# Performance work log

Measured on AMD Instinct MI355X. Metric: run time of the kernel, lower is better.

## Reference

```python
import jax, jax.numpy as jnp
import numpy as np

B, S, D = 2, 400, 512  # batch, seq (src == tgt for self-attention), dim; attn_hidden=0 so d == D


def setup_inputs() -> dict:
    key = jax.random.key(0)
    ks = jax.random.split(key, 9)
    inv = 1.0 / np.sqrt(D)
    return {
        "input": jax.random.normal(ks[0], (B, S, D), jnp.float32),
        "memory_bank": jax.random.normal(ks[1], (B, S, D), jnp.float32),
        # lengths in [S//2, S], guaranteed >= 2 so no row is fully masked
        "memory_lengths": jax.random.randint(ks[2], (B,), S // 2, S + 1, jnp.int32),
        "Wq": jax.random.normal(ks[3], (D, D), jnp.float32) * inv,   # linear_query.weight^T
        "bq": jax.random.normal(ks[4], (D,), jnp.float32) * inv,      # linear_query.bias
        "Wc": jax.random.normal(ks[5], (D, D), jnp.float32) * inv,   # linear_context.weight^T
        "v": jax.random.normal(ks[6], (D,), jnp.float32) * inv,       # v.weight (d -> 1)
        "Wout": jax.random.normal(ks[7], (2 * D, D), jnp.float32) * inv,  # linear_out.weight^T
        "bout": jax.random.normal(ks[8], (D,), jnp.float32) * inv,
    }


def reference(input, memory_bank, memory_lengths, Wq, bq, Wc, v, Wout, bout):
    b, s, d = memory_bank.shape
    # Bahdanau/mlp score: v^T tanh(Wq q + b + Wc h)
    wq = jnp.einsum("btd,de->bte", input, Wq) + bq            # [B,T,d]
    uh = jnp.einsum("bsd,de->bse", memory_bank, Wc)           # [B,S,d]
    wquh = jnp.tanh(wq[:, :, None, :] + uh[:, None, :, :])    # [B,T,S,d] big intermediate
    scores = jnp.einsum("btse,e->bts", wquh, v)               # [B,T,S]
    # padding mask (j < length) with self position masked out on the diagonal
    pos = jnp.arange(s)
    key_mask = pos[None, :] < memory_lengths[:, None]         # [B,S]
    mask = key_mask[:, None, :] & (pos[:, None] != pos[None, :])  # [B,T,S]
    scores = jnp.where(mask, scores, -jnp.inf)
    align = jax.nn.softmax(scores, axis=2)                    # [B,T,S]
    c = jnp.einsum("bts,bsd->btd", align, memory_bank)        # context [B,T,D]
    concat_c = jnp.concatenate([c, input], axis=2)            # [B,T,2D]
    attn_h = jnp.einsum("btf,fd->btd", concat_c, Wout) + bout # [B,T,D]
    # mlp variant: no sigmoid gating
    return attn_h.transpose(1, 0, 2), align.transpose(1, 0, 2)  # [T,B,D], [T,B,S]
```

## Files before the change

kernel.cpp:

```cpp
#include <hip/hip_runtime.h>
#include <math.h>

#define BB 2
#define SS 400
#define DD 512
#define TWO_LOG2E 2.8853900817779268f

#if __has_builtin(__builtin_amdgcn_exp2f)
#define EXP2F(x) __builtin_amdgcn_exp2f(x)
#else
#define EXP2F(x) exp2f(x)
#endif
#define RCPF(x) __builtin_amdgcn_rcpf(x)

#define EAOFF 0
#define MOFF 409600
#define EB4OFF 819200
#define XOFF 1228800
#define PARTCH 320000

typedef __bf16 bf16x8 __attribute__((ext_vector_type(8)));
typedef float floatx16 __attribute__((ext_vector_type(16)));

__global__ __launch_bounds__(256) void k0_prep(
    const float* __restrict__ Wq, const float* __restrict__ Wc,
    const float* __restrict__ Wout, unsigned short* __restrict__ wt)
{
    const int k0 = blockIdx.x * 32;
    const int n0 = blockIdx.y * 32;
    const int g  = blockIdx.z;

    __shared__ float tile[32][33];
    const int nn  = threadIdx.x & 31;
    const int kk0 = threadIdx.x >> 5;
    const int n   = n0 + nn;

    #pragma unroll
    for (int p = 0; p < 4; ++p) {
        const int k = k0 + kk0 + p * 8;
        float val;
        if (n0 < 512) val = (g ? Wc : Wq)[(size_t)k * 512 + n];
        else          val = Wout[((size_t)(g ? k : 512 + k)) * 512 + (n - 512)];
        tile[kk0 + p * 8][nn] = val;
    }
    __syncthreads();

    const int kc = threadIdx.x & 31;
    #pragma unroll
    for (int p = 0; p < 4; ++p) {
        const int nl = (threadIdx.x >> 5) + p * 8;
        const __bf16 h = (__bf16)tile[kc][nl];
        wt[((size_t)(g * 1024 + n0 + nl)) * 512 + k0 + kc] =
            __builtin_bit_cast(unsigned short, h);
    }
}

__global__ __launch_bounds__(64) void k1_mfma(
    const float* __restrict__ input, const float* __restrict__ mb,
    const unsigned short* __restrict__ wt, const float* __restrict__ bq,
    const float* __restrict__ bout, float* __restrict__ ws,
    float* __restrict__ out0)
{
    const int lane = threadIdx.x;
    const int mt   = blockIdx.x;
    const int np   = blockIdx.y;
    const int g    = blockIdx.z;
    const int m    = lane & 31;
    const int kh   = lane >> 5;
    const int n0   = np * 64;

    const float* __restrict__ A = g ? mb : input;
    const float* __restrict__ Arow = A + (size_t)(mt * 32 + m) * 512;
    const unsigned short* __restrict__ w0 =
        wt + ((size_t)(g * 1024 + n0 + m)) * 512 + kh * 8;
    const unsigned short* __restrict__ w1 = w0 + (size_t)32 * 512;

    floatx16 acc0h, acc0l, acc1h, acc1l;
    #pragma unroll
    for (int i = 0; i < 16; ++i) { acc0h[i] = 0.f; acc0l[i] = 0.f;
                                   acc1h[i] = 0.f; acc1l[i] = 0.f; }

    #pragma unroll 4
    for (int ks = 0; ks < 32; ++ks) {
        const int kb = ks * 16 + kh * 8;
        const float4 a0 = *(const float4*)(Arow + kb);
        const float4 a1 = *(const float4*)(Arow + kb + 4);
        const bf16x8 bh0 = *(const bf16x8*)(w0 + ks * 16);
        const bf16x8 bh1 = *(const bf16x8*)(w1 + ks * 16);

        bf16x8 ah, al;
        const float av[8] = {a0.x, a0.y, a0.z, a0.w, a1.x, a1.y, a1.z, a1.w};
        #pragma unroll
        for (int i = 0; i < 8; ++i) {
            const __bf16 h = (__bf16)av[i];
            ah[i] = h;
            al[i] = (__bf16)(av[i] - (float)h);
        }

        acc0h = __builtin_amdgcn_mfma_f32_32x32x16_bf16(ah, bh0, acc0h, 0, 0, 0);
        acc0l = __builtin_amdgcn_mfma_f32_32x32x16_bf16(al, bh0, acc0l, 0, 0, 0);
        acc1h = __builtin_amdgcn_mfma_f32_32x32x16_bf16(ah, bh1, acc1h, 0, 0, 0);
        acc1l = __builtin_amdgcn_mfma_f32_32x32x16_bf16(al, bh1, acc1l, 0, 0, 0);
    }

    const floatx16 c0 = acc0h + acc0l;
    const floatx16 c1 = acc1h + acc1l;
    const int rbase = kh * 4;

    #pragma unroll
    for (int r = 0; r < 16; ++r) {
        const int row  = (r & 3) + 8 * (r >> 2) + rbase;
        const int grow = mt * 32 + row;
        const int bi   = (grow >= SS) ? 1 : 0;
        const int rl   = grow - bi * SS;
        #pragma unroll
        for (int u = 0; u < 2; ++u) {
            const float val  = u ? c1[r] : c0[r];
            const int   gcol = n0 + u * 32 + m;
            if (g == 0) {
                if (gcol < 512) {
                    ws[EAOFF + (size_t)grow * 512 + gcol] =
                        EXP2F(TWO_LOG2E * (val + bq[gcol]));
                } else {
                    const int d = gcol - 512;
                    out0[((size_t)(rl * BB + bi)) * 512 + d] = val + bout[d];
                }
            } else {
                if (gcol < 512) {
                    ws[EB4OFF + (size_t)((bi * 128 + (gcol >> 2)) * SS + rl) * 4
                       + (gcol & 3)] = EXP2F(TWO_LOG2E * val);
                } else {
                    ws[MOFF + (size_t)grow * 512 + (gcol - 512)] = val;
                }
            }
        }
    }
}

__global__ __launch_bounds__(448) void k2a_score(
    const float* __restrict__ ws, const float* __restrict__ v,
    float* __restrict__ part, float* __restrict__ out1)
{
    const int tq = blockIdx.x;
    const int b  = blockIdx.y;
    const int eq = blockIdx.z;
    const int t0 = tq * 4;
    const int s  = threadIdx.x;
    const int sidx = (s < SS) ? s : 0;

    __shared__ float lea[4][128];
    __shared__ float lv[128];
    for (int i = threadIdx.x; i < 512; i += 448)
        lea[i >> 7][i & 127] =
            ws[EAOFF + (size_t)(b * SS + t0 + (i >> 7)) * 512 + eq * 128 + (i & 127)];
    if (threadIdx.x < 128) lv[threadIdx.x] = v[eq * 128 + threadIdx.x];
    __syncthreads();

    const float4* __restrict__ eb4 =
        (const float4*)(ws + EB4OFF) + ((size_t)b * 128 + eq * 32) * SS + sidx;

    float acc[4] = {0.f, 0.f, 0.f, 0.f};
    #pragma unroll 4
    for (int e4 = 0; e4 < 32; ++e4) {
        const float4 eb  = eb4[(size_t)e4 * SS];
        const float4 vv  = *(const float4*)&lv[e4 * 4];
        const float4 ea0 = *(const float4*)&lea[0][e4 * 4];
        const float4 ea1 = *(const float4*)&lea[1][e4 * 4];
        const float4 ea2 = *(const float4*)&lea[2][e4 * 4];
        const float4 ea3 = *(const float4*)&lea[3][e4 * 4];
        #pragma unroll
        for (int j = 0; j < 4; ++j) {
            const float ebv = (&eb.x)[j];
            const float vj  = (&vv.x)[j];
            acc[0] = fmaf(vj, RCPF(fmaf((&ea0.x)[j], ebv, 1.f)), acc[0]);
            acc[1] = fmaf(vj, RCPF(fmaf((&ea1.x)[j], ebv, 1.f)), acc[1]);
            acc[2] = fmaf(vj, RCPF(fmaf((&ea2.x)[j], ebv, 1.f)), acc[2]);
            acc[3] = fmaf(vj, RCPF(fmaf((&ea3.x)[j], ebv, 1.f)), acc[3]);
        }
    }

    if (s < SS) {
        if (eq == 0) {
            #pragma unroll
            for (int t = 0; t < 4; ++t)
                out1[((size_t)((t0 + t) * BB) + b) * SS + s] = -2.f * acc[t];
        } else {
            float* __restrict__ pp = part + (size_t)(eq - 1) * PARTCH
                                   + ((size_t)(b * SS + t0)) * SS + s;
            #pragma unroll
            for (int t = 0; t < 4; ++t)
                pp[(size_t)t * SS] = -2.f * acc[t];
        }
    }
}

__global__ __launch_bounds__(448) void k2b_softmax(
    const float* __restrict__ part, const int* __restrict__ lens,
    float* __restrict__ out1)
{
    const int bt = blockIdx.x;
    const int b  = bt / SS;
    const int t  = bt - b * SS;
    const int tid = threadIdx.x;
    const int s   = tid;
    const int len = lens[b];

    float sc = -INFINITY;
    bool valid = false;
    if (s < SS) {
        valid = (s < len) && (s != t);
        if (valid) {
            const size_t ibts = ((size_t)(t * BB) + b) * SS + s;
            const size_t idx  = (size_t)bt * SS + s;
            sc = out1[ibts] + part[idx]
               + part[PARTCH + idx] + part[2 * (size_t)PARTCH + idx];
        }
    }

    __shared__ float wred[8];
    const int wid  = tid >> 6;
    const int lane = tid & 63;

    float m = sc;
    #pragma unroll
    for (int off = 32; off > 0; off >>= 1) m = fmaxf(m, __shfl_xor(m, off));
    if (lane == 0) wred[wid] = m;
    __syncthreads();
    float mx = wred[0];
    #pragma unroll
    for (int w = 1; w < 7; ++w) mx = fmaxf(mx, wred[w]);
    __syncthreads();

    const float p = valid ? __expf(sc - mx) : 0.f;
    float sm = p;
    #pragma unroll
    for (int off = 32; off > 0; off >>= 1) sm += __shfl_xor(sm, off);
    if (lane == 0) wred[wid] = sm;
    __syncthreads();
    float tot = wred[0];
    #pragma unroll
    for (int w = 1; w < 7; ++w) tot += wred[w];
    const float inv = RCPF(tot);

    if (s < SS) out1[((size_t)(t * BB) + b) * SS + s] = p * inv;
}

__global__ __launch_bounds__(256) void k3_out(
    const float* __restrict__ ws, const float* __restrict__ align_out,
    float* __restrict__ out0)
{
    const int d     = blockIdx.x * 256 + threadIdx.x;
    const int r0    = blockIdx.y * 4;
    const int b     = (r0 >= SS) ? 1 : 0;
    const int tbase = r0 - b * SS;

    const float* __restrict__ Mb = ws + MOFF + (size_t)b * SS * DD;

    float pv[4];
    #pragma unroll
    for (int j = 0; j < 4; ++j)
        pv[j] = out0[((size_t)((tbase + j) * BB) + b) * DD + d];

    float acc[4];
    #pragma unroll
    for (int j = 0; j < 4; ++j) acc[j] = 0.f;

    float mA[4], mB[4];
    float4 alA[4], alB[4];

    auto LOAD = [&](float (&mm)[4], float4 (&al)[4], int s) {
        #pragma unroll
        for (int i = 0; i < 4; ++i)
            mm[i] = Mb[(size_t)(s + i) * DD + d];
        #pragma unroll
        for (int j = 0; j < 4; ++j)
            al[j] = *(const float4*)(align_out +
                     ((size_t)((tbase + j) * BB) + b) * SS + s);
    };
    auto FMA4 = [&](const float (&mm)[4], const float4 (&al)[4]) {
        #pragma unroll
        for (int j = 0; j < 4; ++j) {
            acc[j] = fmaf(al[j].x, mm[0], acc[j]);
            acc[j] = fmaf(al[j].y, mm[1], acc[j]);
            acc[j] = fmaf(al[j].z, mm[2], acc[j]);
            acc[j] = fmaf(al[j].w, mm[3], acc[j]);
        }
    };

    LOAD(mA, alA, 0);
    for (int s = 0; s < SS; s += 8) {
        LOAD(mB, alB, s + 4);
        FMA4(mA, alA);
        if (s + 8 < SS) LOAD(mA, alA, s + 8);
        FMA4(mB, alB);
    }

    #pragma unroll
    for (int j = 0; j < 4; ++j)
        out0[((size_t)((tbase + j) * BB) + b) * DD + d] = acc[j] + pv[j];
}

extern "C" void kernel_launch(void* const* d_in, const int* in_sizes, int n_in,
                              void* d_out, int out_size, void* d_ws, size_t ws_size,
                              hipStream_t stream)
{
    const float* input = (const float*)d_in[0];
    const float* mb    = (const float*)d_in[1];
    const int*   lens  = (const int*)d_in[2];
    const float* Wq    = (const float*)d_in[3];
    const float* bq    = (const float*)d_in[4];
    const float* Wc    = (const float*)d_in[5];
    const float* v     = (const float*)d_in[6];
    const float* Wout  = (const float*)d_in[7];
    const float* bout  = (const float*)d_in[8];

    float* out0 = (float*)d_out;
    float* out1 = out0 + (size_t)BB * SS * DD;
    float* ws   = (float*)d_ws;
    unsigned short* wt = (unsigned short*)(ws + XOFF);
    float* part = ws + XOFF;

    hipLaunchKernelGGL(k0_prep, dim3(16, 32, 2), dim3(256), 0, stream,
                       Wq, Wc, Wout, wt);
    hipLaunchKernelGGL(k1_mfma, dim3(25, 16, 2), dim3(64), 0, stream,
                       input, mb, wt, bq, bout, ws, out0);
    hipLaunchKernelGGL(k2a_score, dim3(100, 2, 4), dim3(448), 0, stream,
                       ws, v, part, out1);
    hipLaunchKernelGGL(k2b_softmax, dim3(800), dim3(448), 0, stream,
                       part, lens, out1);
    hipLaunchKernelGGL(k3_out, dim3(2, 200), dim3(256), 0, stream,
                       ws, out1, out0);
}
```

Baseline: 155.4 us.

## Fuse score and softmax kernels, pre-split activations into bf16 hi/lo

The separate score-partial and softmax kernels are merged into one kernel in which each block handles two query rows over the full 512-wide feature dimension. This removes the partial-sum buffer round trip and one launch. A new pre-pass converts input and memory bank into bf16 high/low halves once, so the MFMA GEMM loads bf16 directly instead of splitting fp32 values inside its inner loop. The trade-off is fewer blocks in the score stage (400 instead of 800), an extra conversion launch, and extra bf16 traffic written and read through the workspace.

Result: no change. 157.0 us (+1.0%).

```diff
diff --git a/kernel.cpp b/kernel.cpp
--- a/kernel.cpp
+++ b/kernel.cpp
@@ -17,7 +17,6 @@
 #define MOFF 409600
 #define EB4OFF 819200
 #define XOFF 1228800
-#define PARTCH 320000
 
 typedef __bf16 bf16x8 __attribute__((ext_vector_type(8)));
 typedef float floatx16 __attribute__((ext_vector_type(16)));
@@ -55,8 +54,28 @@
     }
 }
 
+__global__ __launch_bounds__(256) void k0b_conv(
+    const float* __restrict__ input, const float* __restrict__ mbk,
+    unsigned short* __restrict__ ahi, unsigned short* __restrict__ alo)
+{
+    const int g  = blockIdx.y;
+    const int i4 = blockIdx.x * 256 + threadIdx.x;
+    const float4 a = ((const float4*)(g ? mbk : input))[i4];
+    ushort4 h, l;
+    #pragma unroll
+    for (int j = 0; j < 4; ++j) {
+        const float av = (&a.x)[j];
+        const __bf16 hh = (__bf16)av;
+        (&h.x)[j] = __builtin_bit_cast(unsigned short, hh);
+        const __bf16 ll = (__bf16)(av - (float)hh);
+        (&l.x)[j] = __builtin_bit_cast(unsigned short, ll);
+    }
+    ((ushort4*)(ahi + (size_t)g * 409600))[i4] = h;
+    ((ushort4*)(alo + (size_t)g * 409600))[i4] = l;
+}
+
 __global__ __launch_bounds__(64) void k1_mfma(
-    const float* __restrict__ input, const float* __restrict__ mb,
+    const unsigned short* __restrict__ ahi, const unsigned short* __restrict__ alo,
     const unsigned short* __restrict__ wt, const float* __restrict__ bq,
     const float* __restrict__ bout, float* __restrict__ ws,
     float* __restrict__ out0)
@@ -69,8 +88,9 @@
     const int kh   = lane >> 5;
     const int n0   = np * 64;
 
-    const float* __restrict__ A = g ? mb : input;
-    const float* __restrict__ Arow = A + (size_t)(mt * 32 + m) * 512;
+    const size_t arow = ((size_t)g * 800 + mt * 32 + m) * 512 + kh * 8;
+    const unsigned short* __restrict__ ah = ahi + arow;
+    const unsigned short* __restrict__ al = alo + arow;
     const unsigned short* __restrict__ w0 =
         wt + ((size_t)(g * 1024 + n0 + m)) * 512 + kh * 8;
     const unsigned short* __restrict__ w1 = w0 + (size_t)32 * 512;
@@ -82,25 +102,15 @@
 
     #pragma unroll 4
     for (int ks = 0; ks < 32; ++ks) {
-        const int kb = ks * 16 + kh * 8;
-        const float4 a0 = *(const float4*)(Arow + kb);
-        const float4 a1 = *(const float4*)(Arow + kb + 4);
+        const bf16x8 va0 = *(const bf16x8*)(ah + ks * 16);
+        const bf16x8 va1 = *(const bf16x8*)(al + ks * 16);
         const bf16x8 bh0 = *(const bf16x8*)(w0 + ks * 16);
         const bf16x8 bh1 = *(const bf16x8*)(w1 + ks * 16);
 
-        bf16x8 ah, al;
-        const float av[8] = {a0.x, a0.y, a0.z, a0.w, a1.x, a1.y, a1.z, a1.w};
-        #pragma unroll
-        for (int i = 0; i < 8; ++i) {
-            const __bf16 h = (__bf16)av[i];
-            ah[i] = h;
-            al[i] = (__bf16)(av[i] - (float)h);
-        }
-
-        acc0h = __builtin_amdgcn_mfma_f32_32x32x16_bf16(ah, bh0, acc0h, 0, 0, 0);
-        acc0l = __builtin_amdgcn_mfma_f32_32x32x16_bf16(al, bh0, acc0l, 0, 0, 0);
-        acc1h = __builtin_amdgcn_mfma_f32_32x32x16_bf16(ah, bh1, acc1h, 0, 0, 0);
-        acc1l = __builtin_amdgcn_mfma_f32_32x32x16_bf16(al, bh1, acc1l, 0, 0, 0);
+        acc0h = __builtin_amdgcn_mfma_f32_32x32x16_bf16(va0, bh0, acc0h, 0, 0, 0);
+        acc0l = __builtin_amdgcn_mfma_f32_32x32x16_bf16(va1, bh0, acc0l, 0, 0, 0);
+        acc1h = __builtin_amdgcn_mfma_f32_32x32x16_bf16(va0, bh1, acc1h, 0, 0, 0);
+        acc1l = __builtin_amdgcn_mfma_f32_32x32x16_bf16(va1, bh1, acc1l, 0, 0, 0);
     }
 
     const floatx16 c0 = acc0h + acc0l;
@@ -137,112 +147,91 @@
     }
 }
 
-__global__ __launch_bounds__(448) void k2a_score(
+__global__ __launch_bounds__(448) void k2_attn(
     const float* __restrict__ ws, const float* __restrict__ v,
-    float* __restrict__ part, float* __restrict__ out1)
-{
-    const int tq = blockIdx.x;
+    const int* __restrict__ lens, float* __restrict__ out1)
+{
+    const int tp = blockIdx.x;
     const int b  = blockIdx.y;
-    const int eq = blockIdx.z;
-    const int t0 = tq * 4;
-    const int s  = threadIdx.x;
+    const int t0 = tp * 2;
+    const int t1 = t0 + 1;
+    const int tid = threadIdx.x;
+    const int s   = tid;
     const int sidx = (s < SS) ? s : 0;
-
-    __shared__ float lea[4][128];
-    __shared__ float lv[128];
-    for (int i = threadIdx.x; i < 512; i += 448)
-        lea[i >> 7][i & 127] =
-            ws[EAOFF + (size_t)(b * SS + t0 + (i >> 7)) * 512 + eq * 128 + (i & 127)];
-    if (threadIdx.x < 128) lv[threadIdx.x] = v[eq * 128 + threadIdx.x];
+    const int len  = lens[b];
+
+    __shared__ float lea[2][512];
+    __shared__ float lv[512];
+    for (int i = tid; i < 1024; i += 448)
+        lea[i >> 9][i & 511] =
+            ws[EAOFF + (size_t)(b * SS + t0 + (i >> 9)) * 512 + (i & 511)];
+    for (int i = tid; i < 512; i += 448) lv[i] = v[i];
     __syncthreads();
 
     const float4* __restrict__ eb4 =
-        (const float4*)(ws + EB4OFF) + ((size_t)b * 128 + eq * 32) * SS + sidx;
-
-    float acc[4] = {0.f, 0.f, 0.f, 0.f};
+        (const float4*)(ws + EB4OFF) + (size_t)b * 128 * SS + sidx;
+
+    float acc0 = 0.f, acc1 = 0.f;
     #pragma unroll 4
-    for (int e4 = 0; e4 < 32; ++e4) {
+    for (int e4 = 0; e4 < 128; ++e4) {
         const float4 eb  = eb4[(size_t)e4 * SS];
         const float4 vv  = *(const float4*)&lv[e4 * 4];
         const float4 ea0 = *(const float4*)&lea[0][e4 * 4];
         const float4 ea1 = *(const float4*)&lea[1][e4 * 4];
-        const float4 ea2 = *(const float4*)&lea[2][e4 * 4];
-        const float4 ea3 = *(const float4*)&lea[3][e4 * 4];
         #pragma unroll
         for (int j = 0; j < 4; ++j) {
             const float ebv = (&eb.x)[j];
             const float vj  = (&vv.x)[j];
-            acc[0] = fmaf(vj, RCPF(fmaf((&ea0.x)[j], ebv, 1.f)), acc[0]);
-            acc[1] = fmaf(vj, RCPF(fmaf((&ea1.x)[j], ebv, 1.f)), acc[1]);
-            acc[2] = fmaf(vj, RCPF(fmaf((&ea2.x)[j], ebv, 1.f)), acc[2]);
-            acc[3] = fmaf(vj, RCPF(fmaf((&ea3.x)[j], ebv, 1.f)), acc[3]);
+            acc0 = fmaf(vj, RCPF(fmaf((&ea0.x)[j], ebv, 1.f)), acc0);
+            acc1 = fmaf(vj, RCPF(fmaf((&ea1.x)[j], ebv, 1.f)), acc1);
         }
     }
 
-    if (s < SS) {
-        if (eq == 0) {
-            #pragma unroll
-            for (int t = 0; t < 4; ++t)
-                out1[((size_t)((t0 + t) * BB) + b) * SS + s] = -2.f * acc[t];
-        } else {
-            float* __restrict__ pp = part + (size_t)(eq - 1) * PARTCH
-                                   + ((size_t)(b * SS + t0)) * SS + s;
-            #pragma unroll
-            for (int t = 0; t < 4; ++t)
-                pp[(size_t)t * SS] = -2.f * acc[t];
-        }
-    }
-}
-
-__global__ __launch_bounds__(448) void k2b_softmax(
-    const float* __restrict__ part, const int* __restrict__ lens,
-    float* __restrict__ out1)
-{
-    const int bt = blockIdx.x;
-    const int b  = bt / SS;
-    const int t  = bt - b * SS;
-    const int tid = threadIdx.x;
-    const int s   = tid;
-    const int len = lens[b];
-
-    float sc = -INFINITY;
-    bool valid = false;
-    if (s < SS) {
-        valid = (s < len) && (s != t);
-        if (valid) {
-            const size_t ibts = ((size_t)(t * BB) + b) * SS + s;
-            const size_t idx  = (size_t)bt * SS + s;
-            sc = out1[ibts] + part[idx]
-               + part[PARTCH + idx] + part[2 * (size_t)PARTCH + idx];
-        }
-    }
-
-    __shared__ float wred[8];
+    const bool v0 = (s < SS) && (s < len) && (s != t0);
+    const bool v1 = (s < SS) && (s < len) && (s != t1);
+    const float sc0 = v0 ? -2.f * acc0 : -INFINITY;
+    const float sc1 = v1 ? -2.f * acc1 : -INFINITY;
+
+    __shared__ float wred0[8], wred1[8];
     const int wid  = tid >> 6;
     const int lane = tid & 63;
 
-    float m = sc;
-    #pragma unroll
-    for (int off = 32; off > 0; off >>= 1) m = fmaxf(m, __shfl_xor(m, off));
-    if (lane == 0) wred[wid] = m;
-    __syncthreads();
-    float mx = wred[0];
-    #pragma unroll
-    for (int w = 1; w < 7; ++w) mx = fmaxf(mx, wred[w]);
-    __syncthreads();
-
-    const float p = valid ? __expf(sc - mx) : 0.f;
-    float sm = p;
-    #pragma unroll
-    for (int off = 32; off > 0; off >>= 1) sm += __shfl_xor(sm, off);
-    if (lane == 0) wred[wid] = sm;
-    __syncthreads();
-    float tot = wred[0];
-    #pragma unroll
-    for (int w = 1; w < 7; ++w) tot += wred[w];
-    const float inv = RCPF(tot);
-
-    if (s < SS) out1[((size_t)(t * BB) + b) * SS + s] = p * inv;
+    float m0 = sc0, m1 = sc1;
+    #pragma unroll
+    for (int off = 32; off > 0; off >>= 1) {
+        m0 = fmaxf(m0, __shfl_xor(m0, off));
+        m1 = fmaxf(m1, __shfl_xor(m1, off));
+    }
+    if (lane == 0) { wred0[wid] = m0; wred1[wid] = m1; }
+    __syncthreads();
+    float mx0 = wred0[0], mx1 = wred1[0];
+    #pragma unroll
+    for (int w = 1; w < 7; ++w) {
+        mx0 = fmaxf(mx0, wred0[w]);
+        mx1 = fmaxf(mx1, wred1[w]);
+    }
+    __syncthreads();
+
+    const float p0 = v0 ? __expf(sc0 - mx0) : 0.f;
+    const float p1 = v1 ? __expf(sc1 - mx1) : 0.f;
+    float s0v = p0, s1v = p1;
+    #pragma unroll
+    for (int off = 32; off > 0; off >>= 1) {
+        s0v += __shfl_xor(s0v, off);
+        s1v += __shfl_xor(s1v, off);
+    }
+    if (lane == 0) { wred0[wid] = s0v; wred1[wid] = s1v; }
+    __syncthreads();
+    float tot0 = wred0[0], tot1 = wred1[0];
+    #pragma unroll
+    for (int w = 1; w < 7; ++w) { tot0 += wred0[w]; tot1 += wred1[w]; }
+    const float inv0 = RCPF(tot0);
+    const float inv1 = RCPF(tot1);
+
+    if (s < SS) {
+        out1[((size_t)(t0 * BB) + b) * SS + s] = p0 * inv0;
+        out1[((size_t)(t1 * BB) + b) * SS + s] = p1 * inv1;
+    }
 }
 
 __global__ __launch_bounds__(256) void k3_out(
@@ -305,7 +294,7 @@
                               hipStream_t stream)
 {
     const float* input = (const float*)d_in[0];
-    const float* mb    = (const float*)d_in[1];
+    const float* mbk   = (const float*)d_in[1];
     const int*   lens  = (const int*)d_in[2];
     const float* Wq    = (const float*)d_in[3];
     const float* bq    = (const float*)d_in[4];
@@ -317,17 +306,19 @@
     float* out0 = (float*)d_out;
     float* out1 = out0 + (size_t)BB * SS * DD;
     float* ws   = (float*)d_ws;
-    unsigned short* wt = (unsigned short*)(ws + XOFF);
-    float* part = ws + XOFF;
+    unsigned short* x16 = (unsigned short*)(ws + XOFF);
+    unsigned short* wt  = x16;
+    unsigned short* ahi = x16 + 1048576;
+    unsigned short* alo = ahi + 819200;
 
     hipLaunchKernelGGL(k0_prep, dim3(16, 32, 2), dim3(256), 0, stream,
                        Wq, Wc, Wout, wt);
+    hipLaunchKernelGGL(k0b_conv, dim3(400, 2), dim3(256), 0, stream,
+                       input, mbk, ahi, alo);
     hipLaunchKernelGGL(k1_mfma, dim3(25, 16, 2), dim3(64), 0, stream,
-                       input, mb, wt, bq, bout, ws, out0);
-    hipLaunchKernelGGL(k2a_score, dim3(100, 2, 4), dim3(448), 0, stream,
-                       ws, v, part, out1);
-    hipLaunchKernelGGL(k2b_softmax, dim3(800), dim3(448), 0, stream,
-                       part, lens, out1);
+                       ahi, alo, wt, bq, bout, ws, out0);
+    hipLaunchKernelGGL(k2_attn, dim3(200, 2), dim3(448), 0, stream,
+                       ws, v, lens, out1);
     hipLaunchKernelGGL(k3_out, dim3(2, 200), dim3(256), 0, stream,
                        ws, out1, out0);
 }
```
